# Kernel tuning notes

Measured on AMD Instinct MI355X. Metric: run time of the kernel, lower is better.

## Reference

```python
import jax, jax.numpy as jnp
import numpy as np

N = 65536          # nodes
E = 1048576        # edges (avg degree 16)
K = 5              # B-spline kernel size per dim (dim=3 -> 125 kernels)
F_IN, F_OUT = 1, 32
GRID = 32          # first sparse_voxel_max_pool: size = 1/32 -> 32^3 voxels
NUM_VOX = GRID ** 3

# enumerate the 2^3 corners of the degree-1 B-spline support
_BITS = np.array([[(b >> d) & 1 for d in range(3)] for b in range(8)], dtype=np.int32)  # [8,3]
_STRIDES = np.array([1, K, K * K], dtype=np.int32)  # kernel index strides per dim


def setup_inputs() -> dict:
    key = jax.random.key(0)
    ks = jax.random.split(key, 7)
    x = jax.random.normal(ks[0], (N, F_IN), dtype=jnp.float32)
    edge_index = jax.random.randint(ks[1], (2, E), 0, N, dtype=jnp.int32)
    pseudo = jax.random.uniform(ks[2], (E, 3), dtype=jnp.float32)   # edge pseudo-coords in [0,1]^3
    pos = jax.random.uniform(ks[3], (N, 3), dtype=jnp.float32)      # node positions in [0,1]^3
    W = jax.random.normal(ks[4], (K ** 3, F_IN, F_OUT), dtype=jnp.float32) * 0.1
    W_root = jax.random.normal(ks[5], (F_IN, F_OUT), dtype=jnp.float32) * 0.1
    bias = jax.random.normal(ks[6], (F_OUT,), dtype=jnp.float32) * 0.1
    return {"x": x, "edge_index": edge_index, "pseudo": pseudo, "pos": pos,
            "W": W, "W_root": W_root, "bias": bias}


def spline_basis(pseudo):
    """Degree-1 open B-spline basis. Returns (weights [E,8], kernel_idx [E,8])."""
    v = pseudo * (K - 1)                                   # [E,3] in [0, K-1]
    i0 = jnp.clip(jnp.floor(v), 0, K - 2)                  # lower knot per dim
    f = v - i0                                             # fractional part
    i0 = i0.astype(jnp.int32)
    bits = jnp.asarray(_BITS)                              # [8,3]
    idx = i0[:, None, :] + bits[None]                      # [E,8,3]
    w = jnp.where(bits[None].astype(bool), f[:, None, :], 1.0 - f[:, None, :])
    B = w.prod(axis=-1)                                    # [E,8]
    kidx = (idx * jnp.asarray(_STRIDES)).sum(axis=-1)      # [E,8] in [0,125)
    return B, kidx


def spline_conv(x, edge_index, pseudo, W, W_root, bias):
    src, dst = edge_index[0], edge_index[1]
    B, kidx = spline_basis(pseudo)                         # [E,8], [E,8]
    xj = x[src]                                            # [E,F_IN] edge-wise gather
    Wg = W[kidx]                                           # [E,8,F_IN,F_OUT]
    msg = jnp.einsum('es,ef,esfo->eo', B, xj, Wg)          # basis-weighted messages [E,F_OUT]
    agg = jax.ops.segment_sum(msg, dst, num_segments=N)    # scatter-add
    deg = jax.ops.segment_sum(jnp.ones((E,), jnp.float32), dst, num_segments=N)
    out = agg / jnp.clip(deg, 1.0)[:, None] + x @ W_root + bias  # mean aggr + root + bias
    return out


def reference(x, edge_index, pseudo, pos, W, W_root, bias):
    h = jax.nn.elu(spline_conv(x, edge_index, pseudo, W, W_root, bias))  # [N,32]
    # sparse voxel max pooling: hash positions to a 32^3 grid, scatter-max features
    vid = jnp.clip(jnp.floor(pos * GRID), 0, GRID - 1).astype(jnp.int32)  # [N,3]
    vidx = vid[:, 0] + GRID * vid[:, 1] + GRID * GRID * vid[:, 2]         # [N]
    pooled = jax.ops.segment_max(h, vidx, num_segments=NUM_VOX)           # [32768,32]
    pooled = jnp.where(jnp.isfinite(pooled), pooled, 0.0)                 # empty voxels -> 0
    return pooled
```

## Files before the change

### kernel.cpp

```cpp
#include <hip/hip_runtime.h>
#include <math.h>

#define F_OUT     32
#define GRID_DIM  32
#define NUM_VOX   (GRID_DIM * GRID_DIM * GRID_DIM)

#define NPB   64
#define NBKT  1024
#define SEB   4096
#define SCS   132
#define DEGS  125
#define ECAP  3072

__device__ __forceinline__ unsigned int enc_f32(float f) {
    unsigned int u = __float_as_uint(f);
    return (u & 0x80000000u) ? ~u : (u | 0x80000000u);
}
__device__ __forceinline__ float dec_f32(unsigned int e) {
    return (e & 0x80000000u) ? __uint_as_float(e ^ 0x80000000u)
                             : __uint_as_float(~e);
}

__global__ __launch_bounds__(512) void sort_kernel(
    const int*   __restrict__ src,
    const int*   __restrict__ dst,
    const float* __restrict__ x,
    const float* __restrict__ pseudo,
    float4* __restrict__ payload,
    unsigned int* __restrict__ off_tab,
    int E)
{
    __shared__ unsigned int sHist[NBKT];
    __shared__ unsigned int sStart[NBKT];
    __shared__ unsigned int sWTot[8];
    __shared__ __align__(16) float4 sPay[SEB];

    const int t    = threadIdx.x;
    const int lane = t & 63;
    const int wv   = t >> 6;
    const int e0   = blockIdx.x * SEB;
    const bool full = (e0 + SEB <= E);

    for (int i = t; i < NBKT; i += 512) sHist[i] = 0;
    __syncthreads();

    unsigned short dloc[8];
    float4 pay[8];
    if (full) {
        int   dd[8], ss[8];
        float pp0[8], pp1[8], pp2[8], xj[8];
        #pragma unroll
        for (int i = 0; i < 8; ++i) {
            int e = e0 + i * 512 + t;
            dd[i] = dst[e]; ss[i] = src[e];
            pp0[i] = pseudo[3 * e]; pp1[i] = pseudo[3 * e + 1]; pp2[i] = pseudo[3 * e + 2];
        }
        #pragma unroll
        for (int i = 0; i < 8; ++i) xj[i] = x[ss[i]];
        #pragma unroll
        for (int i = 0; i < 8; ++i) {
            unsigned int q2 = (unsigned int)(pp2[i] * 65535.0f + 0.5f) & 0xFFFFu;
            unsigned int w  = q2 | ((unsigned int)(dd[i] & 63) << 16);
            dloc[i] = (unsigned short)dd[i];
            pay[i]  = make_float4(pp0[i], pp1[i], xj[i], __uint_as_float(w));
            atomicAdd(&sHist[dd[i] >> 6], 1u);
        }
    } else {
        #pragma unroll
        for (int i = 0; i < 8; ++i) {
            int e = e0 + i * 512 + t;
            if (e < E) {
                int d = dst[e];
                float p0 = pseudo[3 * e], p1 = pseudo[3 * e + 1], p2 = pseudo[3 * e + 2];
                float xjv = x[src[e]];
                unsigned int q2 = (unsigned int)(p2 * 65535.0f + 0.5f) & 0xFFFFu;
                unsigned int w  = q2 | ((unsigned int)(d & 63) << 16);
                dloc[i] = (unsigned short)d;
                pay[i]  = make_float4(p0, p1, xjv, __uint_as_float(w));
                atomicAdd(&sHist[d >> 6], 1u);
            } else dloc[i] = 0;
        }
    }
    __syncthreads();

    unsigned int a0 = sHist[2 * t], a1 = sHist[2 * t + 1];
    unsigned int pairSum = a0 + a1;
    unsigned int incl = pairSum;
    #pragma unroll
    for (int d = 1; d < 64; d <<= 1) {
        unsigned int v = __shfl_up(incl, d, 64);
        if (lane >= d) incl += v;
    }
    if (lane == 63) sWTot[wv] = incl;
    __syncthreads();
    unsigned int wofs = 0, total = 0;
    #pragma unroll
    for (int w = 0; w < 8; ++w) {
        unsigned int v = sWTot[w];
        if (w < wv) wofs += v;
        total += v;
    }
    unsigned int ex = wofs + incl - pairSum;
    sStart[2 * t]     = ex;
    sStart[2 * t + 1] = ex + a0;
    sHist[2 * t]      = ex;
    sHist[2 * t + 1]  = ex + a0;
    __syncthreads();

    #pragma unroll
    for (int i = 0; i < 8; ++i) {
        int e = e0 + i * 512 + t;
        if (e < E) {
            unsigned int slot = atomicAdd(&sHist[dloc[i] >> 6], 1u);
            sPay[slot] = pay[i];
        }
    }
    __syncthreads();

    for (unsigned int i = t; i < total; i += 512)
        payload[(size_t)e0 + i] = sPay[i];

    for (int b = t; b < NBKT; b += 512) {
        unsigned int s = sStart[b];
        unsigned int nxt = (b < NBKT - 1) ? sStart[b + 1] : total;
        off_tab[(size_t)blockIdx.x * NBKT + b] = s | ((nxt - s) << 16);
    }
}

__global__ __launch_bounds__(256) void transpose_kernel(
    const unsigned int* __restrict__ in, unsigned int* __restrict__ outT,
    int rows, int cols)
{
    __shared__ unsigned int tile[32][33];
    const int tx = threadIdx.x & 31, ty = threadIdx.x >> 5;
    const int c0 = blockIdx.x * 32, r0 = blockIdx.y * 32;
    #pragma unroll
    for (int r = ty; r < 32; r += 8) {
        int row = r0 + r, col = c0 + tx;
        tile[r][tx] = (row < rows && col < cols) ? in[(size_t)row * cols + col] : 0u;
    }
    __syncthreads();
    #pragma unroll
    for (int r = ty; r < 32; r += 8) {
        int col = c0 + r;
        int row = r0 + tx;
        if (col < cols && row < rows) outT[(size_t)col * rows + row] = tile[tx][r];
    }
}

__device__ __forceinline__ void process_edge(float4 r, float* sC)
{
    float xj = r.z;
    unsigned int w = __float_as_uint(r.w);
    int   rel = (int)((w >> 16) & 63u);
    float p2  = (float)(w & 0xFFFFu) * (1.0f / 65535.0f);

    float v0 = r.x * 4.0f, v1 = r.y * 4.0f, v2 = p2 * 4.0f;
    float i0 = fminf(fmaxf(floorf(v0), 0.0f), 3.0f);
    float i1 = fminf(fmaxf(floorf(v1), 0.0f), 3.0f);
    float i2 = fminf(fmaxf(floorf(v2), 0.0f), 3.0f);
    float f0 = v0 - i0, f1 = v1 - i1, f2 = v2 - i2;
    float g0 = 1.0f - f0, g1 = 1.0f - f1, g2 = 1.0f - f2;
    int k = (int)i0 + 5 * (int)i1 + 25 * (int)i2;

    float w00 = g0 * g1, w10 = f0 * g1, w01 = g0 * f1, w11 = f0 * f1;
    float a2 = xj * g2, b2 = xj * f2;
    float* row = sC + rel * SCS;
    atomicAdd(row + k +  0, w00 * a2);
    atomicAdd(row + k +  1, w10 * a2);
    atomicAdd(row + k +  5, w01 * a2);
    atomicAdd(row + k +  6, w11 * a2);
    atomicAdd(row + k + 25, w00 * b2);
    atomicAdd(row + k + 26, w10 * b2);
    atomicAdd(row + k + 30, w01 * b2);
    atomicAdd(row + k + 31, w11 * b2);
    atomicAdd(row + DEGS, 1.0f);
}

__global__ __launch_bounds__(512) void owner_kernel(
    const float4* __restrict__ payload,
    const unsigned int* __restrict__ off_tabT,
    const float* __restrict__ W,
    const float* __restrict__ x,
    const float* __restrict__ W_root,
    const float* __restrict__ bias,
    float4* __restrict__ h4,
    int Nn, int nSB)
{
    __shared__ __align__(16) float sC[NPB * SCS];
    __shared__ unsigned int sEdge[ECAP];
    __shared__ unsigned int sNe;

    const int t = threadIdx.x;
    const int b = blockIdx.x;
    const int lane = t & 63;

    for (int i = t; i < NPB * SCS / 4; i += 512)
        *(float4*)&sC[i * 4] = make_float4(0.f, 0.f, 0.f, 0.f);
    if (t == 0) sNe = 0;

    unsigned int cnt = 0, start_g = 0;
    if (t < nSB) {
        unsigned int packed = off_tabT[(size_t)b * nSB + t];
        start_g = (unsigned int)t * SEB + (packed & 0xFFFFu);
        cnt = packed >> 16;
    }
    __syncthreads();

    unsigned int incl = cnt;
    #pragma unroll
    for (int d = 1; d < 64; d <<= 1) {
        unsigned int v = __shfl_up(incl, d, 64);
        if (lane >= d) incl += v;
    }
    unsigned int wtot = __shfl(incl, 63, 64);
    unsigned int wbase = 0;
    if (lane == 63 && wtot > 0) wbase = atomicAdd(&sNe, wtot);
    wbase = __shfl(wbase, 63, 64);
    unsigned int off = wbase + incl - cnt;

    for (unsigned int j = 0; j < cnt; ++j) {
        unsigned int p = off + j;
        if (p < ECAP) sEdge[p] = start_g + j;
        else process_edge(payload[start_g + j], sC);
    }
    __syncthreads();

    int ne = (int)sNe; if (ne > ECAP) ne = ECAP;
    for (int i = t; i < ne; i += 1024) {
        float4 r0 = payload[sEdge[i]];
        int j = i + 512;
        bool hj = (j < ne);
        float4 r1 = r0;
        if (hj) r1 = payload[sEdge[j]];
        process_edge(r0, sC);
        if (hj) process_edge(r1, sC);
    }
    __syncthreads();

    const int node = t & 63;
    const int cg   = t >> 6;
    const float* crow = sC + node * SCS;
    float4 acc = make_float4(0.f, 0.f, 0.f, 0.f);
    #pragma unroll 8
    for (int k4 = 0; k4 < 31; ++k4) {
        float4 r = *(const float4*)&crow[k4 * 4];
        const float* wp = W + (k4 * 4) * F_OUT + cg * 4;
        float4 w0 = *(const float4*)(wp);
        float4 w1 = *(const float4*)(wp + F_OUT);
        float4 w2 = *(const float4*)(wp + 2 * F_OUT);
        float4 w3 = *(const float4*)(wp + 3 * F_OUT);
        acc.x += r.x * w0.x + r.y * w1.x + r.z * w2.x + r.w * w3.x;
        acc.y += r.x * w0.y + r.y * w1.y + r.z * w2.y + r.w * w3.y;
        acc.z += r.x * w0.z + r.y * w1.z + r.z * w2.z + r.w * w3.z;
        acc.w += r.x * w0.w + r.y * w1.w + r.z * w2.w + r.w * w3.w;
    }
    {
        float r = crow[124];
        const float* wp = W + 124 * F_OUT + cg * 4;
        acc.x += r * wp[0]; acc.y += r * wp[1];
        acc.z += r * wp[2]; acc.w += r * wp[3];
    }
    float dg = fmaxf(crow[DEGS], 1.0f);
    int   n  = b * NPB + node;
    float xn = (n < Nn) ? x[n] : 0.0f;
    float4 wr = *(const float4*)(W_root + cg * 4);
    float4 bs = *(const float4*)(bias + cg * 4);
    __syncthreads();

    if (n < Nn) {
        float h;
        h = acc.x / dg + xn * wr.x + bs.x; h = h > 0.f ? h : expm1f(h); sC[node * SCS + cg * 4 + 0] = h;
        h = acc.y / dg + xn * wr.y + bs.y; h = h > 0.f ? h : expm1f(h); sC[node * SCS + cg * 4 + 1] = h;
        h = acc.z / dg + xn * wr.z + bs.z; h = h > 0.f ? h : expm1f(h); sC[node * SCS + cg * 4 + 2] = h;
        h = acc.w / dg + xn * wr.w + bs.w; h = h > 0.f ? h : expm1f(h); sC[node * SCS + cg * 4 + 3] = h;
    }
    __syncthreads();

    const int n0 = b * NPB;
    for (int item = t; item < NPB * 8; item += 512) {
        int nr = item >> 3, q = item & 7;
        if (n0 + nr >= Nn) break;
        h4[(size_t)n0 * 8 + item] = *(const float4*)&sC[nr * SCS + q * 4];
    }
}

__global__ __launch_bounds__(256) void voxmax_kernel(
    const float* __restrict__ h,
    const float* __restrict__ pos,
    unsigned int* __restrict__ pooled,
    int Nn)
{
    int gid = blockIdx.x * 256 + threadIdx.x;
    int n = gid >> 5, o = gid & 31;
    if (n >= Nn) return;
    float hv = h[(size_t)n * F_OUT + o];
    int vx = min(max((int)floorf(pos[3 * n + 0] * (float)GRID_DIM), 0), GRID_DIM - 1);
    int vy = min(max((int)floorf(pos[3 * n + 1] * (float)GRID_DIM), 0), GRID_DIM - 1);
    int vz = min(max((int)floorf(pos[3 * n + 2] * (float)GRID_DIM), 0), GRID_DIM - 1);
    int vidx = vx + GRID_DIM * vy + GRID_DIM * GRID_DIM * vz;
    atomicMax(&pooled[(size_t)vidx * F_OUT + o], enc_f32(hv));
}

__global__ __launch_bounds__(256) void finalize_kernel(
    const unsigned int* __restrict__ pooled,
    float* __restrict__ out, int M)
{
    int i = blockIdx.x * blockDim.x + threadIdx.x;
    if (i >= M) return;
    unsigned int u = pooled[i];
    out[i] = (u == 0u) ? 0.0f : dec_f32(u);
}

extern "C" void kernel_launch(void* const* d_in, const int* in_sizes, int n_in,
                              void* d_out, int out_size, void* d_ws, size_t ws_size,
                              hipStream_t stream) {
    const float* x       = (const float*)d_in[0];
    const int*   ei      = (const int*)  d_in[1];
    const float* pseudo  = (const float*)d_in[2];
    const float* pos     = (const float*)d_in[3];
    const float* W       = (const float*)d_in[4];
    const float* W_root  = (const float*)d_in[5];
    const float* bias    = (const float*)d_in[6];
    float* out = (float*)d_out;

    const int E   = in_sizes[1] / 2;
    const int Nn  = in_sizes[0];
    const int nSB = (E + SEB - 1) / SEB;
    const int nb  = (Nn + NPB - 1) / NPB;

    const size_t pooled_b = (size_t)NUM_VOX * F_OUT * 4;
    const size_t off_b    = ((size_t)nSB * NBKT * 4 + 255) & ~(size_t)255;
    const size_t pay_b    = (size_t)nSB * SEB * 16;
    unsigned int* pooled   = (unsigned int*)d_ws;
    unsigned int* off_tab  = (unsigned int*)((char*)d_ws + pooled_b);
    unsigned int* off_tabT = (unsigned int*)((char*)d_ws + pooled_b + off_b);
    float4*       payload  = (float4*)((char*)d_ws + pooled_b + 2 * off_b);
    float4*       h4       = (float4*)((char*)d_ws + pooled_b + 2 * off_b + pay_b);

    hipMemsetAsync(pooled, 0, pooled_b, stream);

    sort_kernel<<<nSB, 512, 0, stream>>>(ei, ei + E, x, pseudo, payload, off_tab, E);
    transpose_kernel<<<dim3((NBKT + 31) / 32, (nSB + 31) / 32), 256, 0, stream>>>(
        off_tab, off_tabT, nSB, NBKT);
    owner_kernel<<<nb, 512, 0, stream>>>(payload, off_tabT, W, x, W_root, bias,
                                         h4, Nn, nSB);
    voxmax_kernel<<<(Nn * F_OUT + 255) / 256, 256, 0, stream>>>(
        (const float*)h4, pos, pooled, Nn);

    const int M = (out_size < NUM_VOX * F_OUT) ? out_size : NUM_VOX * F_OUT;
    finalize_kernel<<<(M + 255) / 256, 256, 0, stream>>>(pooled, out, M);
}
```

Measured before the change: 178.5 us.

## Stage node features in LDS chunks for sort-kernel gather and remap owner threads

```diff
diff --git a/kernel.cpp b/kernel.cpp
--- a/kernel.cpp
+++ b/kernel.cpp
@@ -8,6 +8,7 @@
 #define NPB   64
 #define NBKT  1024
 #define SEB   4096
+#define XQ    16384
 #define SCS   132
 #define DEGS  125
 #define ECAP  3072
@@ -28,58 +29,39 @@
     const float* __restrict__ pseudo,
     float4* __restrict__ payload,
     unsigned int* __restrict__ off_tab,
-    int E)
+    int E, int Nn)
 {
     __shared__ unsigned int sHist[NBKT];
     __shared__ unsigned int sStart[NBKT];
     __shared__ unsigned int sWTot[8];
     __shared__ __align__(16) float4 sPay[SEB];
+    __shared__ __align__(16) float  xq[XQ];
 
     const int t    = threadIdx.x;
     const int lane = t & 63;
     const int wv   = t >> 6;
     const int e0   = blockIdx.x * SEB;
-    const bool full = (e0 + SEB <= E);
 
     for (int i = t; i < NBKT; i += 512) sHist[i] = 0;
     __syncthreads();
 
     unsigned short dloc[8];
+    int   sloc[8];
     float4 pay[8];
-    if (full) {
-        int   dd[8], ss[8];
-        float pp0[8], pp1[8], pp2[8], xj[8];
-        #pragma unroll
-        for (int i = 0; i < 8; ++i) {
-            int e = e0 + i * 512 + t;
-            dd[i] = dst[e]; ss[i] = src[e];
-            pp0[i] = pseudo[3 * e]; pp1[i] = pseudo[3 * e + 1]; pp2[i] = pseudo[3 * e + 2];
-        }
-        #pragma unroll
-        for (int i = 0; i < 8; ++i) xj[i] = x[ss[i]];
-        #pragma unroll
-        for (int i = 0; i < 8; ++i) {
-            unsigned int q2 = (unsigned int)(pp2[i] * 65535.0f + 0.5f) & 0xFFFFu;
-            unsigned int w  = q2 | ((unsigned int)(dd[i] & 63) << 16);
-            dloc[i] = (unsigned short)dd[i];
-            pay[i]  = make_float4(pp0[i], pp1[i], xj[i], __uint_as_float(w));
-            atomicAdd(&sHist[dd[i] >> 6], 1u);
-        }
-    } else {
-        #pragma unroll
-        for (int i = 0; i < 8; ++i) {
-            int e = e0 + i * 512 + t;
-            if (e < E) {
-                int d = dst[e];
-                float p0 = pseudo[3 * e], p1 = pseudo[3 * e + 1], p2 = pseudo[3 * e + 2];
-                float xjv = x[src[e]];
-                unsigned int q2 = (unsigned int)(p2 * 65535.0f + 0.5f) & 0xFFFFu;
-                unsigned int w  = q2 | ((unsigned int)(d & 63) << 16);
-                dloc[i] = (unsigned short)d;
-                pay[i]  = make_float4(p0, p1, xjv, __uint_as_float(w));
-                atomicAdd(&sHist[d >> 6], 1u);
-            } else dloc[i] = 0;
-        }
+    #pragma unroll
+    for (int i = 0; i < 8; ++i) {
+        int e = e0 + i * 512 + t;
+        sloc[i] = -1;
+        if (e < E) {
+            int d = dst[e], s = src[e];
+            float p0 = pseudo[3 * e], p1 = pseudo[3 * e + 1], p2 = pseudo[3 * e + 2];
+            unsigned int q2 = (unsigned int)(p2 * 1023.0f + 0.5f) & 1023u;
+            unsigned int w  = ((unsigned int)s << 16) | ((unsigned int)(d & 63) << 10) | q2;
+            dloc[i] = (unsigned short)d;
+            sloc[i] = s;
+            pay[i]  = make_float4(p0, p1, 0.0f, __uint_as_float(w));
+            atomicAdd(&sHist[d >> 6], 1u);
+        } else dloc[i] = 0;
     }
     __syncthreads();
 
@@ -106,6 +88,31 @@
     sHist[2 * t]      = ex;
     sHist[2 * t + 1]  = ex + a0;
     __syncthreads();
+
+    const float4* x4 = (const float4*)x;
+    for (int q = 0; q < 4; ++q) {
+        for (int i = t; i < XQ / 4; i += 512) {
+            int gi = q * (XQ / 4) + i;
+            float4 v;
+            if ((gi + 1) * 4 <= Nn) v = x4[gi];
+            else {
+                v = make_float4(0.f, 0.f, 0.f, 0.f);
+                int base = gi * 4;
+                if (base + 0 < Nn) v.x = x[base + 0];
+                if (base + 1 < Nn) v.y = x[base + 1];
+                if (base + 2 < Nn) v.z = x[base + 2];
+            }
+            *(float4*)&xq[i * 4] = v;
+        }
+        __syncthreads();
+        #pragma unroll
+        for (int i = 0; i < 8; ++i) {
+            int s = sloc[i];
+            if (s >= 0 && (s >> 14) == q)
+                pay[i].z = xq[s & (XQ - 1)];
+        }
+        __syncthreads();
+    }
 
     #pragma unroll
     for (int i = 0; i < 8; ++i) {
@@ -152,8 +159,8 @@
 {
     float xj = r.z;
     unsigned int w = __float_as_uint(r.w);
-    int   rel = (int)((w >> 16) & 63u);
-    float p2  = (float)(w & 0xFFFFu) * (1.0f / 65535.0f);
+    int   rel = (int)((w >> 10) & 63u);
+    float p2  = (float)(w & 1023u) * (1.0f / 1023.0f);
 
     float v0 = r.x * 4.0f, v1 = r.y * 4.0f, v2 = p2 * 4.0f;
     float i0 = fminf(fmaxf(floorf(v0), 0.0f), 3.0f);
@@ -238,8 +245,8 @@
     }
     __syncthreads();
 
-    const int node = t & 63;
-    const int cg   = t >> 6;
+    const int node = t >> 3;
+    const int cg   = t & 7;
     const float* crow = sC + node * SCS;
     float4 acc = make_float4(0.f, 0.f, 0.f, 0.f);
     #pragma unroll 8
@@ -269,11 +276,11 @@
     __syncthreads();
 
     if (n < Nn) {
-        float h;
-        h = acc.x / dg + xn * wr.x + bs.x; h = h > 0.f ? h : expm1f(h); sC[node * SCS + cg * 4 + 0] = h;
-        h = acc.y / dg + xn * wr.y + bs.y; h = h > 0.f ? h : expm1f(h); sC[node * SCS + cg * 4 + 1] = h;
-        h = acc.z / dg + xn * wr.z + bs.z; h = h > 0.f ? h : expm1f(h); sC[node * SCS + cg * 4 + 2] = h;
-        h = acc.w / dg + xn * wr.w + bs.w; h = h > 0.f ? h : expm1f(h); sC[node * SCS + cg * 4 + 3] = h;
+        float h0 = acc.x / dg + xn * wr.x + bs.x; h0 = h0 > 0.f ? h0 : expm1f(h0);
+        float h1 = acc.y / dg + xn * wr.y + bs.y; h1 = h1 > 0.f ? h1 : expm1f(h1);
+        float h2 = acc.z / dg + xn * wr.z + bs.z; h2 = h2 > 0.f ? h2 : expm1f(h2);
+        float h3 = acc.w / dg + xn * wr.w + bs.w; h3 = h3 > 0.f ? h3 : expm1f(h3);
+        *(float4*)&sC[node * SCS + cg * 4] = make_float4(h0, h1, h2, h3);
     }
     __syncthreads();
 
@@ -340,7 +347,7 @@
 
     hipMemsetAsync(pooled, 0, pooled_b, stream);
 
-    sort_kernel<<<nSB, 512, 0, stream>>>(ei, ei + E, x, pseudo, payload, off_tab, E);
+    sort_kernel<<<nSB, 512, 0, stream>>>(ei, ei + E, x, pseudo, payload, off_tab, E, Nn);
     transpose_kernel<<<dim3((NBKT + 31) / 32, (nSB + 31) / 32), 256, 0, stream>>>(
         off_tab, off_tabT, nSB, NBKT);
     owner_kernel<<<nb, 512, 0, stream>>>(payload, off_tabT, W, x, W_root, bias,
```

Result: slower. 186.4 us (+4.4%).

## Fuse voxel max-pool into owner kernel with persistent grid-stride blocks

Applied to the files above, without the earlier changes.

```diff
diff --git a/kernel.cpp b/kernel.cpp
--- a/kernel.cpp
+++ b/kernel.cpp
@@ -10,7 +10,7 @@
 #define SEB   4096
 #define SCS   132
 #define DEGS  125
-#define ECAP  3072
+#define OWN_BLOCKS 512
 
 __device__ __forceinline__ unsigned int enc_f32(float f) {
     unsigned int u = __float_as_uint(f);
@@ -177,129 +177,104 @@
     atomicAdd(row + DEGS, 1.0f);
 }
 
-__global__ __launch_bounds__(512) void owner_kernel(
+__global__ __launch_bounds__(256) void owner_kernel(
     const float4* __restrict__ payload,
     const unsigned int* __restrict__ off_tabT,
     const float* __restrict__ W,
     const float* __restrict__ x,
     const float* __restrict__ W_root,
     const float* __restrict__ bias,
-    float4* __restrict__ h4,
-    int Nn, int nSB)
-{
-    __shared__ __align__(16) float sC[NPB * SCS];
-    __shared__ unsigned int sEdge[ECAP];
-    __shared__ unsigned int sNe;
-
-    const int t = threadIdx.x;
-    const int b = blockIdx.x;
-    const int lane = t & 63;
-
-    for (int i = t; i < NPB * SCS / 4; i += 512)
-        *(float4*)&sC[i * 4] = make_float4(0.f, 0.f, 0.f, 0.f);
-    if (t == 0) sNe = 0;
-
-    unsigned int cnt = 0, start_g = 0;
-    if (t < nSB) {
-        unsigned int packed = off_tabT[(size_t)b * nSB + t];
-        start_g = (unsigned int)t * SEB + (packed & 0xFFFFu);
-        cnt = packed >> 16;
-    }
-    __syncthreads();
-
-    unsigned int incl = cnt;
-    #pragma unroll
-    for (int d = 1; d < 64; d <<= 1) {
-        unsigned int v = __shfl_up(incl, d, 64);
-        if (lane >= d) incl += v;
-    }
-    unsigned int wtot = __shfl(incl, 63, 64);
-    unsigned int wbase = 0;
-    if (lane == 63 && wtot > 0) wbase = atomicAdd(&sNe, wtot);
-    wbase = __shfl(wbase, 63, 64);
-    unsigned int off = wbase + incl - cnt;
-
-    for (unsigned int j = 0; j < cnt; ++j) {
-        unsigned int p = off + j;
-        if (p < ECAP) sEdge[p] = start_g + j;
-        else process_edge(payload[start_g + j], sC);
-    }
-    __syncthreads();
-
-    int ne = (int)sNe; if (ne > ECAP) ne = ECAP;
-    for (int i = t; i < ne; i += 1024) {
-        float4 r0 = payload[sEdge[i]];
-        int j = i + 512;
-        bool hj = (j < ne);
-        float4 r1 = r0;
-        if (hj) r1 = payload[sEdge[j]];
-        process_edge(r0, sC);
-        if (hj) process_edge(r1, sC);
-    }
-    __syncthreads();
-
-    const int node = t & 63;
-    const int cg   = t >> 6;
-    const float* crow = sC + node * SCS;
-    float4 acc = make_float4(0.f, 0.f, 0.f, 0.f);
-    #pragma unroll 8
-    for (int k4 = 0; k4 < 31; ++k4) {
-        float4 r = *(const float4*)&crow[k4 * 4];
-        const float* wp = W + (k4 * 4) * F_OUT + cg * 4;
-        float4 w0 = *(const float4*)(wp);
-        float4 w1 = *(const float4*)(wp + F_OUT);
-        float4 w2 = *(const float4*)(wp + 2 * F_OUT);
-        float4 w3 = *(const float4*)(wp + 3 * F_OUT);
-        acc.x += r.x * w0.x + r.y * w1.x + r.z * w2.x + r.w * w3.x;
-        acc.y += r.x * w0.y + r.y * w1.y + r.z * w2.y + r.w * w3.y;
-        acc.z += r.x * w0.z + r.y * w1.z + r.z * w2.z + r.w * w3.z;
-        acc.w += r.x * w0.w + r.y * w1.w + r.z * w2.w + r.w * w3.w;
-    }
-    {
-        float r = crow[124];
-        const float* wp = W + 124 * F_OUT + cg * 4;
-        acc.x += r * wp[0]; acc.y += r * wp[1];
-        acc.z += r * wp[2]; acc.w += r * wp[3];
-    }
-    float dg = fmaxf(crow[DEGS], 1.0f);
-    int   n  = b * NPB + node;
-    float xn = (n < Nn) ? x[n] : 0.0f;
-    float4 wr = *(const float4*)(W_root + cg * 4);
-    float4 bs = *(const float4*)(bias + cg * 4);
-    __syncthreads();
-
-    if (n < Nn) {
-        float h;
-        h = acc.x / dg + xn * wr.x + bs.x; h = h > 0.f ? h : expm1f(h); sC[node * SCS + cg * 4 + 0] = h;
-        h = acc.y / dg + xn * wr.y + bs.y; h = h > 0.f ? h : expm1f(h); sC[node * SCS + cg * 4 + 1] = h;
-        h = acc.z / dg + xn * wr.z + bs.z; h = h > 0.f ? h : expm1f(h); sC[node * SCS + cg * 4 + 2] = h;
-        h = acc.w / dg + xn * wr.w + bs.w; h = h > 0.f ? h : expm1f(h); sC[node * SCS + cg * 4 + 3] = h;
-    }
-    __syncthreads();
-
-    const int n0 = b * NPB;
-    for (int item = t; item < NPB * 8; item += 512) {
-        int nr = item >> 3, q = item & 7;
-        if (n0 + nr >= Nn) break;
-        h4[(size_t)n0 * 8 + item] = *(const float4*)&sC[nr * SCS + q * 4];
-    }
-}
-
-__global__ __launch_bounds__(256) void voxmax_kernel(
-    const float* __restrict__ h,
     const float* __restrict__ pos,
     unsigned int* __restrict__ pooled,
-    int Nn)
-{
-    int gid = blockIdx.x * 256 + threadIdx.x;
-    int n = gid >> 5, o = gid & 31;
-    if (n >= Nn) return;
-    float hv = h[(size_t)n * F_OUT + o];
-    int vx = min(max((int)floorf(pos[3 * n + 0] * (float)GRID_DIM), 0), GRID_DIM - 1);
-    int vy = min(max((int)floorf(pos[3 * n + 1] * (float)GRID_DIM), 0), GRID_DIM - 1);
-    int vz = min(max((int)floorf(pos[3 * n + 2] * (float)GRID_DIM), 0), GRID_DIM - 1);
-    int vidx = vx + GRID_DIM * vy + GRID_DIM * GRID_DIM * vz;
-    atomicMax(&pooled[(size_t)vidx * F_OUT + o], enc_f32(hv));
+    int Nn, int nSB, int nb)
+{
+    __shared__ __align__(16) float sC[NPB * SCS];
+
+    const int t = threadIdx.x;
+
+    for (int b = blockIdx.x; b < nb; b += gridDim.x) {
+        for (int i = t; i < NPB * SCS / 4; i += 256)
+            *(float4*)&sC[i * 4] = make_float4(0.f, 0.f, 0.f, 0.f);
+        __syncthreads();
+
+        if (t < nSB) {
+            unsigned int packed = off_tabT[(size_t)b * nSB + t];
+            unsigned int start_g = (unsigned int)t * SEB + (packed & 0xFFFFu);
+            unsigned int cnt = packed >> 16;
+            for (unsigned int j = 0; j < cnt; ++j)
+                process_edge(payload[start_g + j], sC);
+        }
+        __syncthreads();
+
+        const int node = t >> 2;
+        const int cg   = t & 3;
+        const float* crow = sC + node * SCS;
+        float4 accA = make_float4(0.f, 0.f, 0.f, 0.f);
+        float4 accB = make_float4(0.f, 0.f, 0.f, 0.f);
+        #pragma unroll 4
+        for (int k4 = 0; k4 < 31; ++k4) {
+            float4 r = *(const float4*)&crow[k4 * 4];
+            const float* wp = W + (k4 * 4) * F_OUT + cg * 8;
+            float4 a0 = *(const float4*)(wp);
+            float4 b0 = *(const float4*)(wp + 4);
+            float4 a1 = *(const float4*)(wp + F_OUT);
+            float4 b1 = *(const float4*)(wp + F_OUT + 4);
+            float4 a2 = *(const float4*)(wp + 2 * F_OUT);
+            float4 b2 = *(const float4*)(wp + 2 * F_OUT + 4);
+            float4 a3 = *(const float4*)(wp + 3 * F_OUT);
+            float4 b3 = *(const float4*)(wp + 3 * F_OUT + 4);
+            accA.x += r.x * a0.x + r.y * a1.x + r.z * a2.x + r.w * a3.x;
+            accA.y += r.x * a0.y + r.y * a1.y + r.z * a2.y + r.w * a3.y;
+            accA.z += r.x * a0.z + r.y * a1.z + r.z * a2.z + r.w * a3.z;
+            accA.w += r.x * a0.w + r.y * a1.w + r.z * a2.w + r.w * a3.w;
+            accB.x += r.x * b0.x + r.y * b1.x + r.z * b2.x + r.w * b3.x;
+            accB.y += r.x * b0.y + r.y * b1.y + r.z * b2.y + r.w * b3.y;
+            accB.z += r.x * b0.z + r.y * b1.z + r.z * b2.z + r.w * b3.z;
+            accB.w += r.x * b0.w + r.y * b1.w + r.z * b2.w + r.w * b3.w;
+        }
+        {
+            float r = crow[124];
+            const float* wp = W + 124 * F_OUT + cg * 8;
+            accA.x += r * wp[0]; accA.y += r * wp[1];
+            accA.z += r * wp[2]; accA.w += r * wp[3];
+            accB.x += r * wp[4]; accB.y += r * wp[5];
+            accB.z += r * wp[6]; accB.w += r * wp[7];
+        }
+
+        int n = b * NPB + node;
+        if (n < Nn) {
+            float dg = fmaxf(crow[DEGS], 1.0f);
+            float xn = x[n];
+            float4 wrA = *(const float4*)(W_root + cg * 8);
+            float4 wrB = *(const float4*)(W_root + cg * 8 + 4);
+            float4 bsA = *(const float4*)(bias + cg * 8);
+            float4 bsB = *(const float4*)(bias + cg * 8 + 4);
+
+            float h0 = accA.x / dg + xn * wrA.x + bsA.x; h0 = h0 > 0.f ? h0 : expm1f(h0);
+            float h1 = accA.y / dg + xn * wrA.y + bsA.y; h1 = h1 > 0.f ? h1 : expm1f(h1);
+            float h2 = accA.z / dg + xn * wrA.z + bsA.z; h2 = h2 > 0.f ? h2 : expm1f(h2);
+            float h3 = accA.w / dg + xn * wrA.w + bsA.w; h3 = h3 > 0.f ? h3 : expm1f(h3);
+            float h4 = accB.x / dg + xn * wrB.x + bsB.x; h4 = h4 > 0.f ? h4 : expm1f(h4);
+            float h5 = accB.y / dg + xn * wrB.y + bsB.y; h5 = h5 > 0.f ? h5 : expm1f(h5);
+            float h6 = accB.z / dg + xn * wrB.z + bsB.z; h6 = h6 > 0.f ? h6 : expm1f(h6);
+            float h7 = accB.w / dg + xn * wrB.w + bsB.w; h7 = h7 > 0.f ? h7 : expm1f(h7);
+
+            int vx = min(max((int)floorf(pos[3 * n + 0] * (float)GRID_DIM), 0), GRID_DIM - 1);
+            int vy = min(max((int)floorf(pos[3 * n + 1] * (float)GRID_DIM), 0), GRID_DIM - 1);
+            int vz = min(max((int)floorf(pos[3 * n + 2] * (float)GRID_DIM), 0), GRID_DIM - 1);
+            int vidx = vx + GRID_DIM * vy + GRID_DIM * GRID_DIM * vz;
+            unsigned int* pv = pooled + (size_t)vidx * F_OUT + cg * 8;
+            atomicMax(pv + 0, enc_f32(h0));
+            atomicMax(pv + 1, enc_f32(h1));
+            atomicMax(pv + 2, enc_f32(h2));
+            atomicMax(pv + 3, enc_f32(h3));
+            atomicMax(pv + 4, enc_f32(h4));
+            atomicMax(pv + 5, enc_f32(h5));
+            atomicMax(pv + 6, enc_f32(h6));
+            atomicMax(pv + 7, enc_f32(h7));
+        }
+        __syncthreads();
+    }
 }
 
 __global__ __launch_bounds__(256) void finalize_kernel(
@@ -331,22 +306,19 @@
 
     const size_t pooled_b = (size_t)NUM_VOX * F_OUT * 4;
     const size_t off_b    = ((size_t)nSB * NBKT * 4 + 255) & ~(size_t)255;
-    const size_t pay_b    = (size_t)nSB * SEB * 16;
     unsigned int* pooled   = (unsigned int*)d_ws;
     unsigned int* off_tab  = (unsigned int*)((char*)d_ws + pooled_b);
     unsigned int* off_tabT = (unsigned int*)((char*)d_ws + pooled_b + off_b);
     float4*       payload  = (float4*)((char*)d_ws + pooled_b + 2 * off_b);
-    float4*       h4       = (float4*)((char*)d_ws + pooled_b + 2 * off_b + pay_b);
 
     hipMemsetAsync(pooled, 0, pooled_b, stream);
 
     sort_kernel<<<nSB, 512, 0, stream>>>(ei, ei + E, x, pseudo, payload, off_tab, E);
     transpose_kernel<<<dim3((NBKT + 31) / 32, (nSB + 31) / 32), 256, 0, stream>>>(
         off_tab, off_tabT, nSB, NBKT);
-    owner_kernel<<<nb, 512, 0, stream>>>(payload, off_tabT, W, x, W_root, bias,
-                                         h4, Nn, nSB);
-    voxmax_kernel<<<(Nn * F_OUT + 255) / 256, 256, 0, stream>>>(
-        (const float*)h4, pos, pooled, Nn);
+    int grid = (nb < OWN_BLOCKS) ? nb : OWN_BLOCKS;
+    owner_kernel<<<grid, 256, 0, stream>>>(payload, off_tabT, W, x, W_root, bias,
+                                           pos, pooled, Nn, nSB, nb);
 
     const int M = (out_size < NUM_VOX * F_OUT) ? out_size : NUM_VOX * F_OUT;
     finalize_kernel<<<(M + 255) / 256, 256, 0, stream>>>(pooled, out, M);
```

Measured after the change: 194.2 us. +8.8%, slower.
